# Performance work log

Hardware: AMD Instinct MI355X
Metric: run time of the kernel (lower is better)

Reference implementation:

```python
import jax, jax.numpy as jnp
import numpy as np

DIM = 1024
STATE = 256
B, S = 4, 4096

def setup_inputs() -> dict:
    key = jax.random.key(0)
    ks = jax.random.split(key, 8)
    sc_b = 1.0 / np.sqrt(DIM)
    sc_c = 1.0 / np.sqrt(STATE)
    return {
        "x": jax.random.normal(ks[0], (B, S, DIM), dtype=jnp.float32),
        "A": jax.random.normal(ks[1], (STATE,), dtype=jnp.float32) * 0.02,
        "B_w": jax.random.uniform(ks[2], (STATE, DIM), minval=-sc_b, maxval=sc_b),
        "B_b": jax.random.uniform(ks[3], (STATE,), minval=-sc_b, maxval=sc_b),
        "C_w": jax.random.uniform(ks[4], (DIM, STATE), minval=-sc_c, maxval=sc_c),
        "C_b": jax.random.uniform(ks[5], (DIM,), minval=-sc_c, maxval=sc_c),
        "D_w": jax.random.uniform(ks[6], (DIM, DIM), minval=-sc_b, maxval=sc_b),
        "D_b": jax.random.uniform(ks[7], (DIM,), minval=-sc_b, maxval=sc_b),
    }

def reference(x, A, B_w, B_b, C_w, C_b, D_w, D_b):
    # Precompute input projections in batch (the per-step loop only needs state*A + Bu)
    Bu = jnp.einsum('bsd,nd->bsn', x, B_w) + B_b          # [B,S,STATE]
    Du = jnp.einsum('bsd,ed->bse', x, D_w) + D_b          # [B,S,DIM]
    Aexp = jnp.exp(A)[None, :]                             # [1,STATE]
    state0 = jnp.zeros((x.shape[0], A.shape[0]), dtype=x.dtype)

    def step(state, bu_t):
        state = jnp.tanh(state * Aexp + bu_t)
        return state, state

    _, states = jax.lax.scan(step, state0, jnp.swapaxes(Bu, 0, 1))  # [S,B,STATE]
    states = jnp.swapaxes(states, 0, 1)                              # [B,S,STATE]
    y = jnp.einsum('bsn,en->bse', states, C_w) + C_b + Du
    return y
```

## Files before the change

### kernel.cpp

```cpp
#include <hip/hip_runtime.h>
#include <hip/hip_bf16.h>

#define DIM 1024
#define STATE 256
#define BATCH 4
#define SEQ 4096
#define M_TOT (BATCH * SEQ)

typedef short short8 __attribute__((ext_vector_type(8)));
typedef float f32x4 __attribute__((ext_vector_type(4)));

__device__ __forceinline__ unsigned short f2bf(float f) {
  unsigned int u = __float_as_uint(f);
  u += 0x7fff + ((u >> 16) & 1);
  return (unsigned short)(u >> 16);
}

__device__ __forceinline__ void gl_lds16(const void* g, void* l) {
  __builtin_amdgcn_global_load_lds(
      (const __attribute__((address_space(1))) void*)g,
      (__attribute__((address_space(3))) void*)l, 16, 0, 0);
}

#define C2F 2.8853900817779268f
#define LOG2EF 1.4426950408889634f
#define VMC(N) asm volatile("s_waitcnt vmcnt(" #N ")" ::: "memory")

__global__ __launch_bounds__(256) void convert_w(
    const float* __restrict__ A, const float* __restrict__ Bw,
    const float* __restrict__ Bb, const float* __restrict__ Cw,
    const float* __restrict__ Cb, const float* __restrict__ Dw,
    const float* __restrict__ Db, unsigned short* __restrict__ bwb,
    unsigned short* __restrict__ wob, float* __restrict__ bb2,
    float* __restrict__ mP2, float* __restrict__ cbdb) {
  const int bx = blockIdx.x;
  const int t = threadIdx.x;
  if (bx < 256) {
    int c = t * 4;
    const float4 v = *(const float4*)(Bw + (size_t)bx * DIM + c);
    *(ushort4*)(bwb + (size_t)bx * DIM + c) =
        make_ushort4(f2bf(v.x), f2bf(v.y), f2bf(v.z), f2bf(v.w));
  } else if (bx < 256 + 1024) {
    int e = bx - 256;
    if (t < 64) {
      const float4 v = *(const float4*)(Cw + (size_t)e * STATE + t * 4);
      *(ushort4*)(wob + (size_t)e * 1280 + t * 4) =
          make_ushort4(f2bf(v.x), f2bf(v.y), f2bf(v.z), f2bf(v.w));
    }
    const float4 v = *(const float4*)(Dw + (size_t)e * DIM + t * 4);
    *(ushort4*)(wob + (size_t)e * 1280 + 256 + t * 4) =
        make_ushort4(f2bf(v.x), f2bf(v.y), f2bf(v.z), f2bf(v.w));
  } else {
    const float P = C2F * __builtin_amdgcn_exp2f(A[t] * LOG2EF);
    bb2[t] = fmaf(Bb[t], C2F, P);
    mP2[t] = -2.0f * P;
#pragma unroll
    for (int k = 0; k < 4; ++k) {
      const int i = t * 4 + k;
      cbdb[i] = Cb[i] + Db[i];
    }
  }
}

__global__ __launch_bounds__(256, 2) void gemm_GX(
    const float* __restrict__ x,
    const unsigned short* __restrict__ bwb,
    float* __restrict__ G,
    const float* __restrict__ bb2,
    unsigned short* __restrict__ xb)
{
  __shared__ char lds[81920];

  const int tid = threadIdx.x;
  const int wave = tid >> 6;
  const int lane = tid & 63;
  const int lr = lane & 15;
  const int lk = lane >> 4;
  const int m0 = blockIdx.x * 32;

  f32x4 acc[2][4];
#pragma unroll
  for (int i = 0; i < 2; ++i)
#pragma unroll
    for (int j = 0; j < 4; ++j) acc[i][j] = (f32x4){0.f, 0.f, 0.f, 0.f};

  const char* xB  = (const char*)x;
  const char* bwB = (const char*)bwb;
  char* xbB = (char*)xb;

  auto stage = [&](int kt) {
    if (kt >= 32) return;
    char* slot = lds + (kt & 3) * 20480;
    {
      const int r = tid >> 3;
      const int c = (tid & 7) ^ (r & 7);
      gl_lds16(xB + (size_t)(m0 + r) * 4096 + (size_t)kt * 128 + c * 16,
               slot + wave * 1024);
    }
#pragma unroll
    for (int i = 0; i < 4; ++i) {
      const int s = i * 256 + tid;
      const int p = s >> 3;
      const int cp = s & 7;
      const int c = cp ^ (p & 7);
      const int n = 2 * p + (c >> 2);
      const int kc = c & 3;
      gl_lds16(bwB + (size_t)n * 2048 + (size_t)kt * 64 + kc * 16,
               slot + 4096 + i * 4096 + wave * 1024);
    }
  };

  stage(0); stage(1); stage(2);
  VMC(10);
  __builtin_amdgcn_s_barrier();

  for (int t = 0; t < 32; ++t) {
    stage(t + 3);

    const char* As = lds + (t & 3) * 20480;
    const char* Bs = As + 4096;

    short8 af[2], bfr[4];
#pragma unroll
    for (int f = 0; f < 2; ++f) {
      const int row = f * 16 + lr;
      const int sw = row & 7;
      const f32x4 a0 = *(const f32x4*)(As + row * 128 + (((2 * lk)     ^ sw) << 4));
      const f32x4 a1 = *(const f32x4*)(As + row * 128 + (((2 * lk + 1) ^ sw) << 4));
      short8 v;
#pragma unroll
      for (int j = 0; j < 4; ++j) {
        v[j]     = (short)f2bf(a0[j]);
        v[4 + j] = (short)f2bf(a1[j]);
      }
      af[f] = v;
    }
#pragma unroll
    for (int fj = 0; fj < 4; ++fj) {
      const int n = wave * 64 + fj * 16 + lr;
      const int p = n >> 1;
      const int cp = (((n & 1) * 4 + lk)) ^ (p & 7);
      bfr[fj] = *(const short8*)(Bs + p * 128 + (cp << 4));
    }
#pragma unroll
    for (int f = 0; f < 2; ++f)
#pragma unroll
      for (int fj = 0; fj < 4; ++fj)
        acc[f][fj] = __builtin_amdgcn_mfma_f32_16x16x32_bf16(af[f], bfr[fj], acc[f][fj], 0, 0, 0);

    if (((t ^ wave) & 3) == 0) {
#pragma unroll
      for (int f = 0; f < 2; ++f) {
        const int row = f * 16 + lr;
        *(short8*)(xbB + (size_t)(m0 + row) * 2048 + (size_t)t * 64 + lk * 16) = af[f];
      }
    }

    if (t < 31) {
      if (t < 29)       { VMC(10); }
      else if (t == 29) { VMC(5); }
      else              { VMC(0); }
      __builtin_amdgcn_s_barrier();
    }
  }

#pragma unroll
  for (int f = 0; f < 2; ++f)
#pragma unroll
    for (int fj = 0; fj < 4; ++fj)
#pragma unroll
      for (int j = 0; j < 4; ++j) {
        const int rg = m0 + f * 16 + lk * 4 + j;
        const int cg = wave * 64 + fj * 16 + lr;
        G[(size_t)rg * STATE + cg] = fmaf(acc[f][fj][j], C2F, bb2[cg]);
      }
}

__global__ __launch_bounds__(256) void scan_kernel(
    const float* __restrict__ G, const float* __restrict__ mP2arr,
    unsigned short* __restrict__ states) {
  const int b = blockIdx.x >> 6;
  const int chunk = blockIdx.x & 63;
  const int n = threadIdx.x;
  const int t0 = chunk * 64;
  const int start = (t0 > 128) ? (t0 - 128) : 0;
  const int nw = t0 - start;
  const int total = nw + 64;

  const float* g = G + ((size_t)b * SEQ + start) * STATE + n;
  unsigned short* q = states + ((size_t)b * SEQ + start) * STATE + n;
  const float mP2 = mP2arr[n];

  float r = 0.5f;
  constexpr int CH = 16;
  float cur[CH], nxt[CH];
#pragma unroll
  for (int j = 0; j < CH; ++j) cur[j] = g[(size_t)j * STATE];

  const int NC = total / CH;
  for (int c = 0; c < NC; ++c) {
    if (c + 1 < NC) {
      const float* pn = g + (size_t)(c + 1) * CH * STATE;
#pragma unroll
      for (int j = 0; j < CH; ++j) nxt[j] = pn[(size_t)j * STATE];
    }
    if (c * CH >= nw) {
      unsigned short* qc = q + (size_t)c * CH * STATE;
#pragma unroll
      for (int j = 0; j < CH; ++j) {
        const float t = fmaf(mP2, r, cur[j]);
        const float e = __builtin_amdgcn_exp2f(t);
        r = __builtin_amdgcn_rcpf(1.0f + e);
        const float s = fmaf(-2.0f, r, 1.0f);
        qc[(size_t)j * STATE] = f2bf(s);
      }
    } else {
#pragma unroll
      for (int j = 0; j < CH; ++j) {
        const float t = fmaf(mP2, r, cur[j]);
        const float e = __builtin_amdgcn_exp2f(t);
        r = __builtin_amdgcn_rcpf(1.0f + e);
      }
    }
    if (c + 1 < NC) {
#pragma unroll
      for (int j = 0; j < CH; ++j) cur[j] = nxt[j];
    }
  }
}

#define PH(TILE, Q, STG, VMST)                                                 \
  do {                                                                         \
    const char* As = lds + ((TILE) & 1) * 32768;                               \
    const char* Bs = lds + 65536 + ((TILE) & 1) * 32768;                       \
    if ((Q) == 0) {                                                            \
      _Pragma("unroll") for (int fj = 0; fj < 4; ++fj) {                       \
        const int r = wn * 64 + fj * 16 + lr;                                  \
        _Pragma("unroll") for (int kk = 0; kk < 2; ++kk)                       \
          bfr[fj][kk] = *(const short8*)(Bs + r * 128 +                        \
                                         (((kk * 4 + lk) ^ (r & 7)) << 4));    \
      }                                                                        \
    }                                                                          \
    short8 af[2][2];                                                           \
    _Pragma("unroll") for (int fl = 0; fl < 2; ++fl) {                         \
      const int r = wm * 128 + (Q) * 32 + fl * 16 + lr;                        \
      _Pragma("unroll") for (int kk = 0; kk < 2; ++kk)                         \
        af[fl][kk] = *(const short8*)(As + r * 128 +                           \
                                      (((kk * 4 + lk) ^ (r & 7)) << 4));       \
    }                                                                          \
    STG;                                                                       \
    if ((Q) == 0) asm volatile("s_waitcnt lgkmcnt(8)" ::: "memory");           \
    __builtin_amdgcn_s_barrier();                                              \
    __builtin_amdgcn_s_setprio(1);                                             \
    _Pragma("unroll") for (int kk = 0; kk < 2; ++kk)                           \
      _Pragma("unroll") for (int fl = 0; fl < 2; ++fl)                         \
        _Pragma("unroll") for (int fj = 0; fj < 4; ++fj)                       \
          acc[(Q) * 2 + fl][fj] = __builtin_amdgcn_mfma_f32_16x16x32_bf16(     \
              af[fl][kk], bfr[fj][kk], acc[(Q) * 2 + fl][fj], 0, 0, 0);        \
    __builtin_amdgcn_s_setprio(0);                                             \
    VMST;                                                                      \
    __builtin_amdgcn_s_barrier();                                              \
  } while (0)

__global__ __launch_bounds__(512, 2) void gemm_out(
    const unsigned short* __restrict__ stb,
    const unsigned short* __restrict__ xb,
    const unsigned short* __restrict__ wob,
    const float* __restrict__ cbdb,
    float* __restrict__ dout)
{
  __shared__ char lds[131072];

  const int tid = threadIdx.x;
  const int wave = tid >> 6;
  const int lane = tid & 63;
  const int lr = lane & 15;
  const int lk = lane >> 4;
  const int wm = wave >> 2;
  const int wn = wave & 3;

  const int bs = ((blockIdx.x & 7) << 5) | (blockIdx.x >> 3);
  const int m0 = (bs >> 2) * 256;
  const int n0 = (bs & 3) * 256;

  const char* stbB = (const char*)stb;
  const char* xbB  = (const char*)xb;
  const char* wobB = (const char*)wob;

  f32x4 acc[8][4];
#pragma unroll
  for (int i = 0; i < 8; ++i)
#pragma unroll
    for (int j = 0; j < 4; ++j) acc[i][j] = (f32x4){0.f, 0.f, 0.f, 0.f};

  auto stageA = [&](int kt, int h) {
    if (kt >= 20) return;
    const char* base;
    size_t str;
    size_t colb;
    if (kt < 4) { base = stbB; str = 512;  colb = (size_t)kt * 128; }
    else        { base = xbB;  str = 2048; colb = (size_t)(kt - 4) * 128; }
    base += (size_t)m0 * str;
#pragma unroll
    for (int i2 = 0; i2 < 2; ++i2) {
      const int s = i2 * 512 + tid;
      const int r = s >> 3;
      const int cl = (s & 7) ^ (r & 7);
      gl_lds16(base + (size_t)(h * 128 + r) * str + colb + cl * 16,
               lds + ((kt & 1) * 32768) + h * 16384 + i2 * 8192 + wave * 1024);
    }
  };
  auto stageB = [&](int kt, int h) {
    if (kt >= 20) return;
#pragma unroll
    for (int i2 = 0; i2 < 2; ++i2) {
      const int s = i2 * 512 + tid;
      const int r = s >> 3;
      const int cl = (s & 7) ^ (r & 7);
      gl_lds16(wobB + (size_t)(n0 + h * 128 + r) * 2560 + (size_t)kt * 128 + cl * 16,
               lds + 65536 + ((kt & 1) * 32768) + h * 16384 + i2 * 8192 + wave * 1024);
    }
  };

  stageA(0, 0); stageA(0, 1);
  stageB(0, 0); stageB(0, 1);
  stageB(1, 0); stageB(1, 1);
  VMC(4);
  __builtin_amdgcn_s_barrier();

  short8 bfr[4][2];
  for (int i = 0; i < 10; ++i) {
    const int e = 2 * i, o = e + 1;
    PH(e, 0, stageA(o, 0), );
    PH(e, 1, stageA(o, 1), );
    PH(e, 2, stageB(e + 2, 0), );
    PH(e, 3, stageB(e + 2, 1), if (i == 9) { VMC(0); } else { VMC(4); });
    PH(o, 0, stageA(e + 2, 0), );
    PH(o, 1, stageA(e + 2, 1), );
    PH(o, 2, stageB(o + 2, 0), );
    PH(o, 3, stageB(o + 2, 1), VMC(4));
  }

#pragma unroll
  for (int fj = 0; fj < 4; ++fj) {
    const int col = n0 + wn * 64 + fj * 16 + lr;
    const float cb = cbdb[col];
#pragma unroll
    for (int m = 0; m < 8; ++m) {
      const int rowb = m0 + wm * 128 + m * 16 + lk * 4;
#pragma unroll
      for (int j = 0; j < 4; ++j)
        dout[(size_t)(rowb + j) * DIM + col] = acc[m][fj][j] + cb;
    }
  }
}

extern "C" void kernel_launch(void* const* d_in, const int* in_sizes, int n_in,
                              void* d_out, int out_size, void* d_ws, size_t ws_size,
                              hipStream_t stream) {
  const float* x  = (const float*)d_in[0];
  const float* A  = (const float*)d_in[1];
  const float* Bw = (const float*)d_in[2];
  const float* Bb = (const float*)d_in[3];
  const float* Cw = (const float*)d_in[4];
  const float* Cb = (const float*)d_in[5];
  const float* Dw = (const float*)d_in[6];
  const float* Db = (const float*)d_in[7];
  float* dout = (float*)d_out;

  char* ws = (char*)d_ws;
  unsigned short* xb   = (unsigned short*)(ws);
  unsigned short* bwb  = (unsigned short*)(ws + 33554432);
  unsigned short* wob  = (unsigned short*)(ws + 34078720);
  float*          G    = (float*)         (ws + 36700160);
  unsigned short* stb  = (unsigned short*)(ws + 53477376);
  float*          bb2  = (float*)         (ws + 61865984);
  float*          mP2  = (float*)         (ws + 61867008);
  float*          cbdb = (float*)         (ws + 61868032);

  convert_w<<<256 + 1024 + 1, 256, 0, stream>>>(
      A, Bw, Bb, Cw, Cb, Dw, Db, bwb, wob, bb2, mP2, cbdb);
  gemm_GX<<<512, 256, 0, stream>>>(x, bwb, G, bb2, xb);
  scan_kernel<<<BATCH * 64, 256, 0, stream>>>(G, mP2, stb);
  gemm_out<<<256, 512, 0, stream>>>(stb, xb, wob, cbdb, dout);
}
```

Before: 96.10 us.

## Double-buffer B fragments in registers and prefetch next tile during current MFMAs

Replaces the per-phase macro with an explicit schedule in which B fragments for the next k-tile are read from LDS into a second register set, in halves, during phases 2-3 of the current tile. This hides the B-fragment LDS latency that previously stalled phase 0 of each tile. VMEM wait points also move. Output stores become nontemporal to avoid cache pollution. Holding a second B fragment set raises register pressure, which may hurt at 2 blocks per CU.

```diff
diff --git a/kernel.cpp b/kernel.cpp
--- a/kernel.cpp
+++ b/kernel.cpp
@@ -229,39 +229,6 @@
   }
 }
 
-#define PH(TILE, Q, STG, VMST)                                                 \
-  do {                                                                         \
-    const char* As = lds + ((TILE) & 1) * 32768;                               \
-    const char* Bs = lds + 65536 + ((TILE) & 1) * 32768;                       \
-    if ((Q) == 0) {                                                            \
-      _Pragma("unroll") for (int fj = 0; fj < 4; ++fj) {                       \
-        const int r = wn * 64 + fj * 16 + lr;                                  \
-        _Pragma("unroll") for (int kk = 0; kk < 2; ++kk)                       \
-          bfr[fj][kk] = *(const short8*)(Bs + r * 128 +                        \
-                                         (((kk * 4 + lk) ^ (r & 7)) << 4));    \
-      }                                                                        \
-    }                                                                          \
-    short8 af[2][2];                                                           \
-    _Pragma("unroll") for (int fl = 0; fl < 2; ++fl) {                         \
-      const int r = wm * 128 + (Q) * 32 + fl * 16 + lr;                        \
-      _Pragma("unroll") for (int kk = 0; kk < 2; ++kk)                         \
-        af[fl][kk] = *(const short8*)(As + r * 128 +                           \
-                                      (((kk * 4 + lk) ^ (r & 7)) << 4));       \
-    }                                                                          \
-    STG;                                                                       \
-    if ((Q) == 0) asm volatile("s_waitcnt lgkmcnt(8)" ::: "memory");           \
-    __builtin_amdgcn_s_barrier();                                              \
-    __builtin_amdgcn_s_setprio(1);                                             \
-    _Pragma("unroll") for (int kk = 0; kk < 2; ++kk)                           \
-      _Pragma("unroll") for (int fl = 0; fl < 2; ++fl)                         \
-        _Pragma("unroll") for (int fj = 0; fj < 4; ++fj)                       \
-          acc[(Q) * 2 + fl][fj] = __builtin_amdgcn_mfma_f32_16x16x32_bf16(     \
-              af[fl][kk], bfr[fj][kk], acc[(Q) * 2 + fl][fj], 0, 0, 0);        \
-    __builtin_amdgcn_s_setprio(0);                                             \
-    VMST;                                                                      \
-    __builtin_amdgcn_s_barrier();                                              \
-  } while (0)
-
 __global__ __launch_bounds__(512, 2) void gemm_out(
     const unsigned short* __restrict__ stb,
     const unsigned short* __restrict__ xb,
@@ -322,23 +289,75 @@
     }
   };
 
+  short8 bfrE[4][2], bfrO[4][2];
+
+  auto rdA = [&](const char* As, int q, short8 af[2][2]) {
+#pragma unroll
+    for (int fl = 0; fl < 2; ++fl) {
+      const int r = wm * 128 + q * 32 + fl * 16 + lr;
+#pragma unroll
+      for (int kk = 0; kk < 2; ++kk)
+        af[fl][kk] = *(const short8*)(As + r * 128 + (((kk * 4 + lk) ^ (r & 7)) << 4));
+    }
+  };
+  auto rdB2 = [&](const char* Bs, int fj0, short8 bfr[4][2]) {
+#pragma unroll
+    for (int d = 0; d < 2; ++d) {
+      const int fj = fj0 + d;
+      const int r = wn * 64 + fj * 16 + lr;
+#pragma unroll
+      for (int kk = 0; kk < 2; ++kk)
+        bfr[fj][kk] = *(const short8*)(Bs + r * 128 + (((kk * 4 + lk) ^ (r & 7)) << 4));
+    }
+  };
+
+#define MFMAQ(Q, BFR)                                                          \
+  __builtin_amdgcn_s_setprio(1);                                               \
+  _Pragma("unroll") for (int kk = 0; kk < 2; ++kk)                             \
+    _Pragma("unroll") for (int fl = 0; fl < 2; ++fl)                           \
+      _Pragma("unroll") for (int fj = 0; fj < 4; ++fj)                         \
+        acc[(Q) * 2 + fl][fj] = __builtin_amdgcn_mfma_f32_16x16x32_bf16(       \
+            af[fl][kk], BFR[fj][kk], acc[(Q) * 2 + fl][fj], 0, 0, 0);          \
+  __builtin_amdgcn_s_setprio(0)
+
+#define BAR() __builtin_amdgcn_s_barrier()
+
   stageA(0, 0); stageA(0, 1);
   stageB(0, 0); stageB(0, 1);
   stageB(1, 0); stageB(1, 1);
   VMC(4);
-  __builtin_amdgcn_s_barrier();
-
-  short8 bfr[4][2];
+  BAR();
+  rdB2(lds + 65536, 0, bfrE);
+  rdB2(lds + 65536, 2, bfrE);
+
   for (int i = 0; i < 10; ++i) {
     const int e = 2 * i, o = e + 1;
-    PH(e, 0, stageA(o, 0), );
-    PH(e, 1, stageA(o, 1), );
-    PH(e, 2, stageB(e + 2, 0), );
-    PH(e, 3, stageB(e + 2, 1), if (i == 9) { VMC(0); } else { VMC(4); });
-    PH(o, 0, stageA(e + 2, 0), );
-    PH(o, 1, stageA(e + 2, 1), );
-    PH(o, 2, stageB(o + 2, 0), );
-    PH(o, 3, stageB(o + 2, 1), VMC(4));
+    const char* Ase = lds + (e & 1) * 32768;
+    const char* Aso = lds + (o & 1) * 32768;
+    const char* Bso = lds + 65536 + (o & 1) * 32768;
+    const char* Bse2 = lds + 65536 + (e & 1) * 32768;
+    short8 af[2][2];
+
+    rdA(Ase, 0, af); stageA(o, 0);
+    BAR(); MFMAQ(0, bfrE); BAR();
+    rdA(Ase, 1, af); stageA(o, 1);
+    BAR(); MFMAQ(1, bfrE); VMC(4); BAR();
+    rdA(Ase, 2, af); rdB2(Bso, 0, bfrO); stageB(e + 2, 0);
+    BAR(); MFMAQ(2, bfrE); BAR();
+    rdA(Ase, 3, af); rdB2(Bso, 2, bfrO); stageB(e + 2, 1);
+    BAR(); MFMAQ(3, bfrE); VMC(4); BAR();
+    rdA(Aso, 0, af); stageA(e + 2, 0);
+    BAR(); MFMAQ(0, bfrO); BAR();
+    rdA(Aso, 1, af); stageA(e + 2, 1);
+    BAR(); MFMAQ(1, bfrO); VMC(4); BAR();
+    rdA(Aso, 2, af);
+    if (i < 9) rdB2(Bse2, 0, bfrE);
+    stageB(o + 2, 0);
+    BAR(); MFMAQ(2, bfrO); BAR();
+    rdA(Aso, 3, af);
+    if (i < 9) rdB2(Bse2, 2, bfrE);
+    stageB(o + 2, 1);
+    BAR(); MFMAQ(3, bfrO); VMC(4); BAR();
   }
 
 #pragma unroll
@@ -350,9 +369,12 @@
       const int rowb = m0 + wm * 128 + m * 16 + lk * 4;
 #pragma unroll
       for (int j = 0; j < 4; ++j)
-        dout[(size_t)(rowb + j) * DIM + col] = acc[m][fj][j] + cb;
+        __builtin_nontemporal_store(acc[m][fj][j] + cb,
+                                    &dout[(size_t)(rowb + j) * DIM + col]);
     }
   }
+#undef MFMAQ
+#undef BAR
 }
 
 extern "C" void kernel_launch(void* const* d_in, const int* in_sizes, int n_in,
```

Result: slower. 101.5 us (+5.6%).
